# Kernel optimization log

Hardware: AMD Instinct MI355X
Metric: run time of the kernel (lower is better)

Reference implementation:

```python
import jax, jax.numpy as jnp
import numpy as np

N = 100000      # nodes
E = 3200000     # edges (avg degree 32)
D_IN, H, D_OUT = 512, 16, 64


def setup_inputs() -> dict:
    key = jax.random.key(0)
    k = jax.random.split(key, 7)
    x = jax.random.normal(k[0], (N, D_IN), dtype=jnp.float32)
    edge_index = jax.random.randint(k[1], (2, E), 0, N, dtype=jnp.int64)
    edge_weight = jax.random.uniform(k[2], (E,), dtype=jnp.float32)
    W1 = jax.random.normal(k[3], (D_IN, H), dtype=jnp.float32) * (1.0 / np.sqrt(D_IN))
    b1 = jnp.zeros((H,), dtype=jnp.float32)
    W2 = jax.random.normal(k[4], (H, D_OUT), dtype=jnp.float32) * (1.0 / np.sqrt(H))
    b2 = jnp.zeros((D_OUT,), dtype=jnp.float32)
    return {"x": x, "edge_index": edge_index, "edge_weight": edge_weight,
            "W1": W1, "b1": b1, "W2": W2, "b2": b2}


def _gcn_conv(x, edge_index, edge_weight, W, b):
    """PyG GCNConv (normalize=True, add self-loops): D^-1/2 (A+I) D^-1/2 (x W) + b."""
    n = x.shape[0]
    src, dst = edge_index[0], edge_index[1]
    loop = jnp.arange(n, dtype=src.dtype)
    row = jnp.concatenate([src, loop])            # message source
    col = jnp.concatenate([dst, loop])            # aggregation target
    w = jnp.concatenate([edge_weight, jnp.ones((n,), x.dtype)])
    deg = jax.ops.segment_sum(w, col, num_segments=n)
    dinv = jnp.where(deg > 0, jax.lax.rsqrt(deg), 0.0)
    norm = dinv[row] * w * dinv[col]              # [E+N]
    h = x @ W                                     # linear before propagate (PyG order)
    msg = h[row] * norm[:, None]                  # gather + scale, [E+N, d_out]
    out = jax.ops.segment_sum(msg, col, num_segments=n)  # scatter-add
    return out + b


def reference(x, edge_index, edge_weight, W1, b1, W2, b2):
    h = jax.nn.relu(_gcn_conv(x, edge_index, edge_weight, W1, b1))
    # F.dropout(training=self.training): identity in eval mode
    return _gcn_conv(h, edge_index, edge_weight, W2, b2)
```

## Files before the change

### kernel.cpp

```cpp
#include <hip/hip_runtime.h>


constexpr int BKT_BITS = 8;
constexpr int BKT = 1 << BKT_BITS;
constexpr int EPB = 16384;

__global__ __launch_bounds__(256) void k_pre(
    const float* __restrict__ x, const float* __restrict__ W1,
    float* __restrict__ h1pre, int n,
    const int* __restrict__ dst, int* __restrict__ hist, int ne, int nb,
    int xw1b) {
  __shared__ float W1t[16 * 512];
  if ((int)blockIdx.x >= xw1b) {
    int* sh = (int*)W1t;
    int hb = blockIdx.x - xw1b;
    for (int i = threadIdx.x; i < nb; i += 256) sh[i] = 0;
    __syncthreads();
    int base = hb * EPB;
    int end = min(base + EPB, ne);
    for (int e = base + threadIdx.x; e < end; e += 256)
      atomicAdd(&sh[dst[e] >> BKT_BITS], 1);
    __syncthreads();
    for (int i = threadIdx.x; i < nb; i += 256) hist[hb * nb + i] = sh[i];
    return;
  }
  {
#pragma unroll
    for (int i = 0; i < 32; ++i) {
      int idx = threadIdx.x + i * 256;
      int k = idx >> 4, j = idx & 15;
      W1t[j * 512 + k] = W1[idx];
    }
  }
  __syncthreads();
  int gtid = blockIdx.x * 256 + threadIdx.x;
  int rp = gtid >> 2, q = gtid & 3;
  int r0 = rp * 2;
  if (r0 >= n) return;
  int r1 = r0 + 1;
  bool has1 = (r1 < n);
  const float4* x4 = (const float4*)x;
  const float4* W1t4 = (const float4*)W1t;
  float acc0[16], acc1[16];
#pragma unroll
  for (int j = 0; j < 16; ++j) { acc0[j] = 0.f; acc1[j] = 0.f; }
  long rb0 = (long)r0 * 128 + q;
  long rb1 = (long)r1 * 128 + q;
  for (int m = 0; m < 32; ++m) {
    float4 a = x4[rb0 + m * 4];
    float4 b = has1 ? x4[rb1 + m * 4] : make_float4(0.f, 0.f, 0.f, 0.f);
    int p = q + m * 4;
#pragma unroll
    for (int j = 0; j < 16; ++j) {
      float4 w = W1t4[j * 128 + p];
      acc0[j] = fmaf(a.x, w.x, acc0[j]);
      acc0[j] = fmaf(a.y, w.y, acc0[j]);
      acc0[j] = fmaf(a.z, w.z, acc0[j]);
      acc0[j] = fmaf(a.w, w.w, acc0[j]);
      acc1[j] = fmaf(b.x, w.x, acc1[j]);
      acc1[j] = fmaf(b.y, w.y, acc1[j]);
      acc1[j] = fmaf(b.z, w.z, acc1[j]);
      acc1[j] = fmaf(b.w, w.w, acc1[j]);
    }
  }
#pragma unroll
  for (int j = 0; j < 16; ++j) {
    acc0[j] += __shfl_xor(acc0[j], 1);
    acc0[j] += __shfl_xor(acc0[j], 2);
    acc1[j] += __shfl_xor(acc1[j], 1);
    acc1[j] += __shfl_xor(acc1[j], 2);
  }
  if (q == 0) {
    float4* o4 = (float4*)h1pre;
#pragma unroll
    for (int j4 = 0; j4 < 4; ++j4) {
      o4[(long)r0 * 4 + j4] =
          make_float4(acc0[4 * j4], acc0[4 * j4 + 1], acc0[4 * j4 + 2], acc0[4 * j4 + 3]);
      if (has1)
        o4[(long)r1 * 4 + j4] =
            make_float4(acc1[4 * j4], acc1[4 * j4 + 1], acc1[4 * j4 + 2], acc1[4 * j4 + 3]);
    }
  }
}

__global__ __launch_bounds__(256) void k_colscan(
    const int* __restrict__ hist, int* __restrict__ basep,
    int* __restrict__ colsum, int nblk, int nb) {
  __shared__ int sh[256];
  __shared__ int carry_s;
  int k = blockIdx.x;
  int t = threadIdx.x;
  if (t == 0) carry_s = 0;
  __syncthreads();
  for (int c0 = 0; c0 < nblk; c0 += 256) {
    int b = c0 + t;
    int v = (b < nblk) ? hist[b * nb + k] : 0;
    sh[t] = v;
    __syncthreads();
    for (int d = 1; d < 256; d <<= 1) {
      int u = (t >= d) ? sh[t - d] : 0;
      __syncthreads();
      sh[t] += u;
      __syncthreads();
    }
    if (b < nblk) basep[b * nb + k] = carry_s + sh[t] - v;
    __syncthreads();
    if (t == 0) carry_s += sh[255];
    __syncthreads();
  }
  if (t == 0) colsum[k] = carry_s;
}

__global__ __launch_bounds__(256) void k_scanb(
    const int* __restrict__ colsum, int* __restrict__ bstart, int nb) {
  __shared__ int sh[256];
  __shared__ int carry_s;
  int t = threadIdx.x;
  if (t == 0) carry_s = 0;
  __syncthreads();
  for (int c0 = 0; c0 < nb; c0 += 256) {
    int k = c0 + t;
    int v = (k < nb) ? colsum[k] : 0;
    sh[t] = v;
    __syncthreads();
    for (int d = 1; d < 256; d <<= 1) {
      int u = (t >= d) ? sh[t - d] : 0;
      __syncthreads();
      sh[t] += u;
      __syncthreads();
    }
    if (k < nb) bstart[k] = carry_s + sh[t] - v;
    __syncthreads();
    if (t == 0) carry_s += sh[255];
    __syncthreads();
  }
  if (t == 0) bstart[nb] = carry_s;
}

__global__ __launch_bounds__(256) void k_binfill(
    const int* __restrict__ ei, const float* __restrict__ ew,
    const int* __restrict__ basep, const int* __restrict__ bstart,
    uint2* __restrict__ recs, int ne, int nb) {
  extern __shared__ int cur[];
  for (int i = threadIdx.x; i < nb; i += 256)
    cur[i] = basep[blockIdx.x * nb + i] + bstart[i];
  __syncthreads();
  int bs = blockIdx.x * EPB;
  int end = min(bs + EPB, ne);
  for (int e = bs + threadIdx.x; e < end; e += 256) {
    int s = ei[e];
    int d = ei[ne + e];
    float w = ew[e];
    int bkt = d >> BKT_BITS;
    int pos = atomicAdd(&cur[bkt], 1);
    recs[pos] = make_uint2((unsigned)s | ((unsigned)(d & (BKT - 1)) << 20),
                           __float_as_uint(w));
  }
}

__global__ __launch_bounds__(256) void k_csr(
    const uint2* __restrict__ recs, const int* __restrict__ bstart,
    uint2* __restrict__ csr, int* __restrict__ rowptr,
    float* __restrict__ dinv, float* __restrict__ h1pre, int n, int ne) {
  __shared__ float sdeg[BKT];
  __shared__ int soff[BKT];
  __shared__ int scur[BKT];
  int t = threadIdx.x;
  sdeg[t] = 0.f;
  soff[t] = 0;
  __syncthreads();
  int k = blockIdx.x;
  int s0 = bstart[k], s1 = bstart[k + 1];
  for (int e = s0 + t; e < s1; e += 256) {
    uint2 r = recs[e];
    int dl = (r.x >> 20) & (BKT - 1);
    atomicAdd(&soff[dl], 1);
    atomicAdd(&sdeg[dl], __uint_as_float(r.y));
  }
  __syncthreads();
  int v = soff[t];
  for (int d = 1; d < BKT; d <<= 1) {
    int u = (t >= d) ? soff[t - d] : 0;
    __syncthreads();
    soff[t] += u;
    __syncthreads();
  }
  int excl = soff[t] - v;
  scur[t] = excl;
  int node = (k << BKT_BITS) + t;
  float dvv = 0.f;
  if (node < n) {
    dvv = 1.0f / sqrtf(sdeg[t] + 1.0f);
    rowptr[node] = s0 + excl;
    dinv[node] = dvv;
  }
  sdeg[t] = dvv;
  if (k == 0 && t == 0) rowptr[n] = ne;
  __syncthreads();
  for (int e = s0 + t; e < s1; e += 256) {
    uint2 r = recs[e];
    int dl = (r.x >> 20) & (BKT - 1);
    int pos = s0 + atomicAdd(&scur[dl], 1);
    csr[pos] = make_uint2(r.x & 0xFFFFF, r.y);
  }
  int nbase = k << BKT_BITS;
  int lim4 = (min(n - nbase, BKT)) * 4;
  float4* h4 = (float4*)h1pre + (long)nbase * 4;
  for (int i = t; i < lim4; i += 256) {
    float dv2 = sdeg[i >> 2];
    float4 hv = h4[i];
    hv.x *= dv2; hv.y *= dv2; hv.z *= dv2; hv.w *= dv2;
    h4[i] = hv;
  }
}

template <int MODE>
__global__ __launch_bounds__(256) void k_agg(
    const float* __restrict__ hin, const uint2* __restrict__ csr,
    const int* __restrict__ rowptr, const float* __restrict__ dinv,
    const float* __restrict__ bias, const float* __restrict__ W2,
    float* __restrict__ out, int n) {
  __shared__ float W2s[MODE == 2 ? 16 * 64 : 1];
  __shared__ float accs[MODE == 2 ? 64 * 16 : 1];
  if (MODE == 2) {
#pragma unroll
    for (int s = 0; s < 4; ++s) W2s[threadIdx.x + s * 256] = W2[threadIdx.x + s * 256];
  }
  const float4* hin4 = (const float4*)hin;
  int gtid = blockIdx.x * 256 + threadIdx.x;
  int node = gtid >> 2, q = gtid & 3;
  bool valid = node < n;
  float4 acc = make_float4(0.f, 0.f, 0.f, 0.f);
  float dv = 0.f;
  if (valid) {
    dv = dinv[node];
    acc = hin4[(long)node * 4 + q];
    int e = rowptr[node], e1 = rowptr[node + 1];
    for (; e + 3 < e1; e += 4) {
      uint2 r0 = csr[e], r1 = csr[e + 1], r2 = csr[e + 2], r3 = csr[e + 3];
      float4 h0 = hin4[(long)r0.x * 4 + q];
      float4 h1 = hin4[(long)r1.x * 4 + q];
      float4 h2 = hin4[(long)r2.x * 4 + q];
      float4 h3 = hin4[(long)r3.x * 4 + q];
      float f0 = __uint_as_float(r0.y), f1 = __uint_as_float(r1.y);
      float f2 = __uint_as_float(r2.y), f3 = __uint_as_float(r3.y);
      acc.x = fmaf(f0, h0.x, acc.x); acc.y = fmaf(f0, h0.y, acc.y);
      acc.z = fmaf(f0, h0.z, acc.z); acc.w = fmaf(f0, h0.w, acc.w);
      acc.x = fmaf(f1, h1.x, acc.x); acc.y = fmaf(f1, h1.y, acc.y);
      acc.z = fmaf(f1, h1.z, acc.z); acc.w = fmaf(f1, h1.w, acc.w);
      acc.x = fmaf(f2, h2.x, acc.x); acc.y = fmaf(f2, h2.y, acc.y);
      acc.z = fmaf(f2, h2.z, acc.z); acc.w = fmaf(f2, h2.w, acc.w);
      acc.x = fmaf(f3, h3.x, acc.x); acc.y = fmaf(f3, h3.y, acc.y);
      acc.z = fmaf(f3, h3.z, acc.z); acc.w = fmaf(f3, h3.w, acc.w);
    }
    for (; e < e1; ++e) {
      uint2 r = csr[e];
      float4 h = hin4[(long)r.x * 4 + q];
      float f = __uint_as_float(r.y);
      acc.x = fmaf(f, h.x, acc.x); acc.y = fmaf(f, h.y, acc.y);
      acc.z = fmaf(f, h.z, acc.z); acc.w = fmaf(f, h.w, acc.w);
    }
    acc.x *= dv; acc.y *= dv; acc.z *= dv; acc.w *= dv;
  }
  if (MODE == 1) {
    if (valid) {
      float4 b = ((const float4*)bias)[q];
      float4 o;
      o.x = dv * fmaxf(acc.x + b.x, 0.f);
      o.y = dv * fmaxf(acc.y + b.y, 0.f);
      o.z = dv * fmaxf(acc.z + b.z, 0.f);
      o.w = dv * fmaxf(acc.w + b.w, 0.f);
      ((float4*)out)[(long)node * 4 + q] = o;
    }
    return;
  }
  ((float4*)accs)[threadIdx.x] = acc;
  __syncthreads();
  const float4* W2s4 = (const float4*)W2s;
#pragma unroll
  for (int it = 0; it < 4; ++it) {
    int nl = it * 16 + (threadIdx.x >> 4);
    int o4 = threadIdx.x & 15;
    int node2 = blockIdx.x * 64 + nl;
    if (node2 < n) {
      float4 v = ((const float4*)bias)[o4];
#pragma unroll
      for (int jj = 0; jj < 16; ++jj) {
        float a = accs[nl * 16 + jj];
        float4 w = W2s4[jj * 16 + o4];
        v.x = fmaf(a, w.x, v.x);
        v.y = fmaf(a, w.y, v.y);
        v.z = fmaf(a, w.z, v.z);
        v.w = fmaf(a, w.w, v.w);
      }
      ((float4*)out)[(long)node2 * 16 + o4] = v;
    }
  }
}

extern "C" void kernel_launch(void* const* d_in, const int* in_sizes, int n_in,
                              void* d_out, int out_size, void* d_ws, size_t ws_size,
                              hipStream_t stream) {
  const float* x  = (const float*)d_in[0];
  const int*   ei = (const int*)d_in[1];
  const float* ew = (const float*)d_in[2];
  const float* W1 = (const float*)d_in[3];
  const float* b1 = (const float*)d_in[4];
  const float* W2 = (const float*)d_in[5];
  const float* b2 = (const float*)d_in[6];
  float* out = (float*)d_out;
  int n  = in_sizes[0] / 512;
  int ne = in_sizes[1] / 2;

  int nb   = (n + BKT - 1) >> BKT_BITS;
  int nblk = (ne + EPB - 1) / EPB;

  char* ws = (char*)d_ws;
  size_t off = 0;
  auto alloc = [&](size_t bytes) {
    size_t r = off;
    off += (bytes + 255) & ~(size_t)255;
    return r;
  };
  float* dinv   = (float*)(ws + alloc((size_t)n * 4));
  float* h1pre  = (float*)(ws + alloc((size_t)n * 16 * 4));
  float* h1     = (float*)(ws + alloc((size_t)n * 16 * 4));
  uint2* recs   = (uint2*)(ws + alloc((size_t)ne * 8));
  uint2* csr    = (uint2*)(ws + alloc((size_t)ne * 8));
  int*   rowptr = (int*)  (ws + alloc((size_t)(n + 1) * 4));
  int*   hist   = (int*)  (ws + alloc((size_t)nblk * nb * 4));
  int*   basep  = (int*)  (ws + alloc((size_t)nblk * nb * 4));
  int*   colsum = (int*)  (ws + alloc((size_t)nb * 4));
  int*   bstart = (int*)  (ws + alloc((size_t)(nb + 1) * 4));
  (void)ws_size; (void)n_in; (void)out_size;

  int nrp = (n + 1) / 2;
  int xw1b = (nrp * 4 + 255) / 256;
  k_pre<<<xw1b + nblk, 256, 0, stream>>>(x, W1, h1pre, n, ei + ne, hist, ne, nb, xw1b);

  k_colscan<<<nb, 256, 0, stream>>>(hist, basep, colsum, nblk, nb);
  k_scanb<<<1, 256, 0, stream>>>(colsum, bstart, nb);
  size_t shb = (size_t)nb * 4;
  k_binfill<<<nblk, 256, shb, stream>>>(ei, ew, basep, bstart, recs, ne, nb);
  k_csr<<<nb, 256, 0, stream>>>(recs, bstart, csr, rowptr, dinv, h1pre, n, ne);

  int gN4 = (n * 4 + 255) / 256;
  k_agg<1><<<gN4, 256, 0, stream>>>(h1pre, csr, rowptr, dinv, b1, nullptr, h1, n);
  k_agg<2><<<gN4, 256, 0, stream>>>(h1, csr, rowptr, dinv, b2, W2, out, n);
}
```

Measured before the change: 260.7 us.

## Store gathered node features as fp16 and deepen edge-gather unroll with nontemporal loads

The pre-scaled first-layer features and the hidden activations are now stored as half2, which halves the bytes moved by the random neighbour gathers in both aggregation passes. The aggregation loop is unrolled to eight edges, and the CSR records are read with nontemporal loads so they do not evict the feature arrays from cache. EPB is also halved, doubling the number of histogram and binning blocks. The cost is fp16 rounding error in the intermediate features, which could matter for tolerance.

After: 270.2 us. 1.04x slower.

```diff
diff --git a/kernel.cpp b/kernel.cpp
--- a/kernel.cpp
+++ b/kernel.cpp
@@ -1,9 +1,14 @@
 #include <hip/hip_runtime.h>
+#include <hip/hip_fp16.h>
 
 
 constexpr int BKT_BITS = 8;
 constexpr int BKT = 1 << BKT_BITS;
-constexpr int EPB = 16384;
+constexpr int EPB = 8192;
+
+__device__ __forceinline__ unsigned long long nt_load_u64(const void* p) {
+  return __builtin_nontemporal_load((const unsigned long long*)p);
+}
 
 __global__ __launch_bounds__(256) void k_pre(
     const float* __restrict__ x, const float* __restrict__ W1,
@@ -161,7 +166,8 @@
 __global__ __launch_bounds__(256) void k_csr(
     const uint2* __restrict__ recs, const int* __restrict__ bstart,
     uint2* __restrict__ csr, int* __restrict__ rowptr,
-    float* __restrict__ dinv, float* __restrict__ h1pre, int n, int ne) {
+    float* __restrict__ dinv, const float* __restrict__ h1pre,
+    __half2* __restrict__ hp16, int n, int ne) {
   __shared__ float sdeg[BKT];
   __shared__ int soff[BKT];
   __shared__ int scur[BKT];
@@ -204,29 +210,31 @@
     csr[pos] = make_uint2(r.x & 0xFFFFF, r.y);
   }
   int nbase = k << BKT_BITS;
-  int lim4 = (min(n - nbase, BKT)) * 4;
-  float4* h4 = (float4*)h1pre + (long)nbase * 4;
-  for (int i = t; i < lim4; i += 256) {
-    float dv2 = sdeg[i >> 2];
-    float4 hv = h4[i];
-    hv.x *= dv2; hv.y *= dv2; hv.z *= dv2; hv.w *= dv2;
-    h4[i] = hv;
+  int nn = min(n - nbase, BKT);
+  if (nn > 0) {
+    const float2* hf2 = (const float2*)h1pre + (long)nbase * 8;
+    __half2* hp2 = hp16 + (long)nbase * 8;
+    int lim2 = nn * 8;
+    for (int i = t; i < lim2; i += 256) {
+      float dv2 = sdeg[i >> 3];
+      float2 hv = hf2[i];
+      hp2[i] = __floats2half2_rn(hv.x * dv2, hv.y * dv2);
+    }
   }
 }
 
 template <int MODE>
 __global__ __launch_bounds__(256) void k_agg(
-    const float* __restrict__ hin, const uint2* __restrict__ csr,
+    const __half2* __restrict__ hin2, const uint2* __restrict__ csr,
     const int* __restrict__ rowptr, const float* __restrict__ dinv,
     const float* __restrict__ bias, const float* __restrict__ W2,
-    float* __restrict__ out, int n) {
+    void* __restrict__ outv, int n) {
   __shared__ float W2s[MODE == 2 ? 16 * 64 : 1];
   __shared__ float accs[MODE == 2 ? 64 * 16 : 1];
   if (MODE == 2) {
 #pragma unroll
     for (int s = 0; s < 4; ++s) W2s[threadIdx.x + s * 256] = W2[threadIdx.x + s * 256];
   }
-  const float4* hin4 = (const float4*)hin;
   int gtid = blockIdx.x * 256 + threadIdx.x;
   int node = gtid >> 2, q = gtid & 3;
   bool valid = node < n;
@@ -234,49 +242,65 @@
   float dv = 0.f;
   if (valid) {
     dv = dinv[node];
-    acc = hin4[(long)node * 4 + q];
+    int hb = (node << 3) + (q << 1);
+    {
+      float2 f0 = __half22float2(hin2[hb]);
+      float2 f1 = __half22float2(hin2[hb + 1]);
+      acc = make_float4(f0.x, f0.y, f1.x, f1.y);
+    }
     int e = rowptr[node], e1 = rowptr[node + 1];
-    for (; e + 3 < e1; e += 4) {
-      uint2 r0 = csr[e], r1 = csr[e + 1], r2 = csr[e + 2], r3 = csr[e + 3];
-      float4 h0 = hin4[(long)r0.x * 4 + q];
-      float4 h1 = hin4[(long)r1.x * 4 + q];
-      float4 h2 = hin4[(long)r2.x * 4 + q];
-      float4 h3 = hin4[(long)r3.x * 4 + q];
-      float f0 = __uint_as_float(r0.y), f1 = __uint_as_float(r1.y);
-      float f2 = __uint_as_float(r2.y), f3 = __uint_as_float(r3.y);
-      acc.x = fmaf(f0, h0.x, acc.x); acc.y = fmaf(f0, h0.y, acc.y);
-      acc.z = fmaf(f0, h0.z, acc.z); acc.w = fmaf(f0, h0.w, acc.w);
-      acc.x = fmaf(f1, h1.x, acc.x); acc.y = fmaf(f1, h1.y, acc.y);
-      acc.z = fmaf(f1, h1.z, acc.z); acc.w = fmaf(f1, h1.w, acc.w);
-      acc.x = fmaf(f2, h2.x, acc.x); acc.y = fmaf(f2, h2.y, acc.y);
-      acc.z = fmaf(f2, h2.z, acc.z); acc.w = fmaf(f2, h2.w, acc.w);
-      acc.x = fmaf(f3, h3.x, acc.x); acc.y = fmaf(f3, h3.y, acc.y);
-      acc.z = fmaf(f3, h3.z, acc.z); acc.w = fmaf(f3, h3.w, acc.w);
+    for (; e + 7 < e1; e += 8) {
+      unsigned long long rv[8];
+#pragma unroll
+      for (int u = 0; u < 8; ++u) rv[u] = nt_load_u64(&csr[e + u]);
+      float2 g0[8], g1[8];
+      float wv[8];
+#pragma unroll
+      for (int u = 0; u < 8; ++u) {
+        int src = (int)(unsigned)rv[u];
+        wv[u] = __uint_as_float((unsigned)(rv[u] >> 32));
+        int b = (src << 3) + (q << 1);
+        g0[u] = __half22float2(hin2[b]);
+        g1[u] = __half22float2(hin2[b + 1]);
+      }
+#pragma unroll
+      for (int u = 0; u < 8; ++u) {
+        acc.x = fmaf(wv[u], g0[u].x, acc.x);
+        acc.y = fmaf(wv[u], g0[u].y, acc.y);
+        acc.z = fmaf(wv[u], g1[u].x, acc.z);
+        acc.w = fmaf(wv[u], g1[u].y, acc.w);
+      }
     }
     for (; e < e1; ++e) {
-      uint2 r = csr[e];
-      float4 h = hin4[(long)r.x * 4 + q];
-      float f = __uint_as_float(r.y);
-      acc.x = fmaf(f, h.x, acc.x); acc.y = fmaf(f, h.y, acc.y);
-      acc.z = fmaf(f, h.z, acc.z); acc.w = fmaf(f, h.w, acc.w);
+      unsigned long long rv = nt_load_u64(&csr[e]);
+      int src = (int)(unsigned)rv;
+      float w = __uint_as_float((unsigned)(rv >> 32));
+      int b = (src << 3) + (q << 1);
+      float2 f0 = __half22float2(hin2[b]);
+      float2 f1 = __half22float2(hin2[b + 1]);
+      acc.x = fmaf(w, f0.x, acc.x);
+      acc.y = fmaf(w, f0.y, acc.y);
+      acc.z = fmaf(w, f1.x, acc.z);
+      acc.w = fmaf(w, f1.y, acc.w);
     }
     acc.x *= dv; acc.y *= dv; acc.z *= dv; acc.w *= dv;
   }
   if (MODE == 1) {
     if (valid) {
       float4 b = ((const float4*)bias)[q];
-      float4 o;
-      o.x = dv * fmaxf(acc.x + b.x, 0.f);
-      o.y = dv * fmaxf(acc.y + b.y, 0.f);
-      o.z = dv * fmaxf(acc.z + b.z, 0.f);
-      o.w = dv * fmaxf(acc.w + b.w, 0.f);
-      ((float4*)out)[(long)node * 4 + q] = o;
+      __half2* o2 = (__half2*)outv;
+      int hb = (node << 3) + (q << 1);
+      o2[hb] = __floats2half2_rn(dv * fmaxf(acc.x + b.x, 0.f),
+                                 dv * fmaxf(acc.y + b.y, 0.f));
+      o2[hb + 1] = __floats2half2_rn(dv * fmaxf(acc.z + b.z, 0.f),
+                                     dv * fmaxf(acc.w + b.w, 0.f));
     }
     return;
   }
   ((float4*)accs)[threadIdx.x] = acc;
   __syncthreads();
   const float4* W2s4 = (const float4*)W2s;
+  float* out = (float*)outv;
 #pragma unroll
   for (int it = 0; it < 4; ++it) {
     int nl = it * 16 + (threadIdx.x >> 4);
@@ -322,16 +346,17 @@
     off += (bytes + 255) & ~(size_t)255;
     return r;
   };
-  float* dinv   = (float*)(ws + alloc((size_t)n * 4));
-  float* h1pre  = (float*)(ws + alloc((size_t)n * 16 * 4));
-  float* h1     = (float*)(ws + alloc((size_t)n * 16 * 4));
-  uint2* recs   = (uint2*)(ws + alloc((size_t)ne * 8));
-  uint2* csr    = (uint2*)(ws + alloc((size_t)ne * 8));
-  int*   rowptr = (int*)  (ws + alloc((size_t)(n + 1) * 4));
-  int*   hist   = (int*)  (ws + alloc((size_t)nblk * nb * 4));
-  int*   basep  = (int*)  (ws + alloc((size_t)nblk * nb * 4));
-  int*   colsum = (int*)  (ws + alloc((size_t)nb * 4));
-  int*   bstart = (int*)  (ws + alloc((size_t)(nb + 1) * 4));
+  float*   dinv   = (float*)  (ws + alloc((size_t)n * 4));
+  float*   h1pre  = (float*)  (ws + alloc((size_t)n * 16 * 4));
+  __half2* hp16   = (__half2*)(ws + alloc((size_t)n * 16 * 2));
+  __half2* h1p16  = (__half2*)(ws + alloc((size_t)n * 16 * 2));
+  uint2*   recs   = (uint2*)  (ws + alloc((size_t)ne * 8));
+  uint2*   csr    = (uint2*)  (ws + alloc((size_t)ne * 8));
+  int*     rowptr = (int*)    (ws + alloc((size_t)(n + 1) * 4));
+  int*     hist   = (int*)    (ws + alloc((size_t)nblk * nb * 4));
+  int*     basep  = (int*)    (ws + alloc((size_t)nblk * nb * 4));
+  int*     colsum = (int*)    (ws + alloc((size_t)nb * 4));
+  int*     bstart = (int*)    (ws + alloc((size_t)(nb + 1) * 4));
   (void)ws_size; (void)n_in; (void)out_size;
 
   int nrp = (n + 1) / 2;
@@ -342,9 +367,9 @@
   k_scanb<<<1, 256, 0, stream>>>(colsum, bstart, nb);
   size_t shb = (size_t)nb * 4;
   k_binfill<<<nblk, 256, shb, stream>>>(ei, ew, basep, bstart, recs, ne, nb);
-  k_csr<<<nb, 256, 0, stream>>>(recs, bstart, csr, rowptr, dinv, h1pre, n, ne);
+  k_csr<<<nb, 256, 0, stream>>>(recs, bstart, csr, rowptr, dinv, h1pre, hp16, n, ne);
 
   int gN4 = (n * 4 + 255) / 256;
-  k_agg<1><<<gN4, 256, 0, stream>>>(h1pre, csr, rowptr, dinv, b1, nullptr, h1, n);
-  k_agg<2><<<gN4, 256, 0, stream>>>(h1, csr, rowptr, dinv, b2, W2, out, n);
-}
+  k_agg<1><<<gN4, 256, 0, stream>>>(hp16, csr, rowptr, dinv, b1, nullptr, h1p16, n);
+  k_agg<2><<<gN4, 256, 0, stream>>>(h1p16, csr, rowptr, dinv, b2, W2, out, n);
+}
```

## Shrink sort buckets and fuse bucket-start scan into column scan via last-block ticket

Applied to the files above, without the earlier changes.

Reduces the bucket size from 256 to 64 nodes and the edges per histogram block from 16384 to 8192. This spreads the CSR build across more blocks with less shared-memory atomic contention per bucket. The separate single-block bucket-start scan kernel is folded into the column-scan kernel: the last block to finish, found with an atomic ticket counter, performs the final scan, which saves one launch. The per-bucket prefix scan in the CSR kernel now uses wave shuffles instead of a shared-memory loop. In exchange there are more histogram entries to scan (nb×nblk grows about eightfold), and the fused scan relies on fence and atomic ordering.

Result: slower. 474.0 us (+81.8%).

```diff
diff --git a/kernel.cpp b/kernel.cpp
--- a/kernel.cpp
+++ b/kernel.cpp
@@ -1,16 +1,17 @@
 #include <hip/hip_runtime.h>
 
 
-constexpr int BKT_BITS = 8;
+constexpr int BKT_BITS = 6;
 constexpr int BKT = 1 << BKT_BITS;
-constexpr int EPB = 16384;
+constexpr int EPB = 8192;
 
 __global__ __launch_bounds__(256) void k_pre(
     const float* __restrict__ x, const float* __restrict__ W1,
     float* __restrict__ h1pre, int n,
     const int* __restrict__ dst, int* __restrict__ hist, int ne, int nb,
-    int xw1b) {
+    int xw1b, int* __restrict__ donecnt) {
   __shared__ float W1t[16 * 512];
+  if (blockIdx.x == 0 && threadIdx.x == 0) *donecnt = 0;
   if ((int)blockIdx.x >= xw1b) {
     int* sh = (int*)W1t;
     int hb = blockIdx.x - xw1b;
@@ -85,9 +86,11 @@
 
 __global__ __launch_bounds__(256) void k_colscan(
     const int* __restrict__ hist, int* __restrict__ basep,
-    int* __restrict__ colsum, int nblk, int nb) {
+    int* __restrict__ colsum, int* __restrict__ bstart,
+    int* __restrict__ donecnt, int nblk, int nb) {
   __shared__ int sh[256];
   __shared__ int carry_s;
+  __shared__ int is_last;
   int k = blockIdx.x;
   int t = threadIdx.x;
   if (t == 0) carry_s = 0;
@@ -108,19 +111,20 @@
     if (t == 0) carry_s += sh[255];
     __syncthreads();
   }
-  if (t == 0) colsum[k] = carry_s;
-}
-
-__global__ __launch_bounds__(256) void k_scanb(
-    const int* __restrict__ colsum, int* __restrict__ bstart, int nb) {
-  __shared__ int sh[256];
-  __shared__ int carry_s;
-  int t = threadIdx.x;
+  if (t == 0) atomicExch(&colsum[k], carry_s);
+  __threadfence();
+  if (t == 0) {
+    int ticket = atomicAdd(donecnt, 1);
+    is_last = (ticket == (int)gridDim.x - 1);
+  }
+  __syncthreads();
+  if (!is_last) return;
+  __threadfence();
   if (t == 0) carry_s = 0;
   __syncthreads();
   for (int c0 = 0; c0 < nb; c0 += 256) {
-    int k = c0 + t;
-    int v = (k < nb) ? colsum[k] : 0;
+    int kk = c0 + t;
+    int v = (kk < nb) ? atomicAdd(&colsum[kk], 0) : 0;
     sh[t] = v;
     __syncthreads();
     for (int d = 1; d < 256; d <<= 1) {
@@ -129,7 +133,7 @@
       sh[t] += u;
       __syncthreads();
     }
-    if (k < nb) bstart[k] = carry_s + sh[t] - v;
+    if (kk < nb) bstart[kk] = carry_s + sh[t] - v;
     __syncthreads();
     if (t == 0) carry_s += sh[255];
     __syncthreads();
@@ -163,39 +167,40 @@
     uint2* __restrict__ csr, int* __restrict__ rowptr,
     float* __restrict__ dinv, float* __restrict__ h1pre, int n, int ne) {
   __shared__ float sdeg[BKT];
-  __shared__ int soff[BKT];
+  __shared__ int scnt[BKT];
   __shared__ int scur[BKT];
   int t = threadIdx.x;
-  sdeg[t] = 0.f;
-  soff[t] = 0;
+  if (t < BKT) { sdeg[t] = 0.f; scnt[t] = 0; }
   __syncthreads();
   int k = blockIdx.x;
   int s0 = bstart[k], s1 = bstart[k + 1];
   for (int e = s0 + t; e < s1; e += 256) {
     uint2 r = recs[e];
     int dl = (r.x >> 20) & (BKT - 1);
-    atomicAdd(&soff[dl], 1);
+    atomicAdd(&scnt[dl], 1);
     atomicAdd(&sdeg[dl], __uint_as_float(r.y));
   }
   __syncthreads();
-  int v = soff[t];
-  for (int d = 1; d < BKT; d <<= 1) {
-    int u = (t >= d) ? soff[t - d] : 0;
-    __syncthreads();
-    soff[t] += u;
-    __syncthreads();
-  }
-  int excl = soff[t] - v;
-  scur[t] = excl;
-  int node = (k << BKT_BITS) + t;
-  float dvv = 0.f;
-  if (node < n) {
-    dvv = 1.0f / sqrtf(sdeg[t] + 1.0f);
-    rowptr[node] = s0 + excl;
-    dinv[node] = dvv;
-  }
-  sdeg[t] = dvv;
-  if (k == 0 && t == 0) rowptr[n] = ne;
+  if (t < BKT) {
+    int v = scnt[t];
+    int incl = v;
+#pragma unroll
+    for (int d = 1; d < BKT; d <<= 1) {
+      int u = __shfl_up(incl, d);
+      if (t >= d) incl += u;
+    }
+    int excl = incl - v;
+    scur[t] = excl;
+    int node = (k << BKT_BITS) + t;
+    float dvv = 0.f;
+    if (node < n) {
+      dvv = 1.0f / sqrtf(sdeg[t] + 1.0f);
+      rowptr[node] = s0 + excl;
+      dinv[node] = dvv;
+    }
+    sdeg[t] = dvv;
+    if (k == 0 && t == 0) rowptr[n] = ne;
+  }
   __syncthreads();
   for (int e = s0 + t; e < s1; e += 256) {
     uint2 r = recs[e];
@@ -204,13 +209,13 @@
     csr[pos] = make_uint2(r.x & 0xFFFFF, r.y);
   }
   int nbase = k << BKT_BITS;
-  int lim4 = (min(n - nbase, BKT)) * 4;
-  float4* h4 = (float4*)h1pre + (long)nbase * 4;
-  for (int i = t; i < lim4; i += 256) {
-    float dv2 = sdeg[i >> 2];
-    float4 hv = h4[i];
+  int lim4 = min(n - nbase, BKT) * 4;
+  if (t < lim4) {
+    float dv2 = sdeg[t >> 2];
+    float4* h4 = (float4*)h1pre + (long)nbase * 4;
+    float4 hv = h4[t];
     hv.x *= dv2; hv.y *= dv2; hv.z *= dv2; hv.w *= dv2;
-    h4[i] = hv;
+    h4[t] = hv;
   }
 }
 
@@ -322,24 +327,25 @@
     off += (bytes + 255) & ~(size_t)255;
     return r;
   };
-  float* dinv   = (float*)(ws + alloc((size_t)n * 4));
-  float* h1pre  = (float*)(ws + alloc((size_t)n * 16 * 4));
-  float* h1     = (float*)(ws + alloc((size_t)n * 16 * 4));
-  uint2* recs   = (uint2*)(ws + alloc((size_t)ne * 8));
-  uint2* csr    = (uint2*)(ws + alloc((size_t)ne * 8));
-  int*   rowptr = (int*)  (ws + alloc((size_t)(n + 1) * 4));
-  int*   hist   = (int*)  (ws + alloc((size_t)nblk * nb * 4));
-  int*   basep  = (int*)  (ws + alloc((size_t)nblk * nb * 4));
-  int*   colsum = (int*)  (ws + alloc((size_t)nb * 4));
-  int*   bstart = (int*)  (ws + alloc((size_t)(nb + 1) * 4));
+  float* dinv    = (float*)(ws + alloc((size_t)n * 4));
+  float* h1pre   = (float*)(ws + alloc((size_t)n * 16 * 4));
+  float* h1      = (float*)(ws + alloc((size_t)n * 16 * 4));
+  uint2* recs    = (uint2*)(ws + alloc((size_t)ne * 8));
+  uint2* csr     = (uint2*)(ws + alloc((size_t)ne * 8));
+  int*   rowptr  = (int*)  (ws + alloc((size_t)(n + 1) * 4));
+  int*   hist    = (int*)  (ws + alloc((size_t)nblk * nb * 4));
+  int*   basep   = (int*)  (ws + alloc((size_t)nblk * nb * 4));
+  int*   colsum  = (int*)  (ws + alloc((size_t)nb * 4));
+  int*   bstart  = (int*)  (ws + alloc((size_t)(nb + 1) * 4));
+  int*   donecnt = (int*)  (ws + alloc(4));
   (void)ws_size; (void)n_in; (void)out_size;
 
   int nrp = (n + 1) / 2;
   int xw1b = (nrp * 4 + 255) / 256;
-  k_pre<<<xw1b + nblk, 256, 0, stream>>>(x, W1, h1pre, n, ei + ne, hist, ne, nb, xw1b);
-
-  k_colscan<<<nb, 256, 0, stream>>>(hist, basep, colsum, nblk, nb);
-  k_scanb<<<1, 256, 0, stream>>>(colsum, bstart, nb);
+  k_pre<<<xw1b + nblk, 256, 0, stream>>>(x, W1, h1pre, n, ei + ne, hist, ne, nb,
+                                         xw1b, donecnt);
+
+  k_colscan<<<nb, 256, 0, stream>>>(hist, basep, colsum, bstart, donecnt, nblk, nb);
   size_t shb = (size_t)nb * 4;
   k_binfill<<<nblk, 256, shb, stream>>>(ei, ew, basep, bstart, recs, ne, nb);
   k_csr<<<nb, 256, 0, stream>>>(recs, bstart, csr, rowptr, dinv, h1pre, n, ne);
```
